# Kernel tuning notes

Measured on AMD Instinct MI355X. Metric: run time of the kernel, lower is better.

Reference implementation:

```python
import jax, jax.numpy as jnp
import numpy as np

B, S, F, H = 64, 1024, 128, 512  # batch, seq_len, features, lstm units


def setup_inputs() -> dict:
    key = jax.random.key(0)
    k1, k2, k3 = jax.random.split(key, 3)
    x = jax.random.normal(k1, (B, S, F), dtype=jnp.float32)
    # Keras LSTM params: kernel [F, 4H], recurrent_kernel [H, 4H], bias [4H]
    W = jax.random.normal(k2, (F, 4 * H), dtype=jnp.float32) * (1.0 / np.sqrt(F))
    U = jax.random.normal(k3, (H, 4 * H), dtype=jnp.float32) * (1.0 / np.sqrt(H))
    b = jnp.zeros((4 * H,), dtype=jnp.float32)
    return {"x": x, "W": W, "U": U, "b": b}


def _lstm_relu(x, W, U, b):
    # Precompute input projection for all timesteps: [B,S,4H]
    xW = jnp.einsum("bsf,fg->bsg", x, W) + b
    xW_t = jnp.transpose(xW, (1, 0, 2))  # [S,B,4H] for scan over time
    h0 = jnp.zeros((x.shape[0], H), dtype=x.dtype)
    c0 = jnp.zeros((x.shape[0], H), dtype=x.dtype)

    def step(carry, xw):
        h, c = carry
        z = xw + h @ U  # [B,4H]
        zi, zf, zg, zo = jnp.split(z, 4, axis=-1)  # Keras gate order i,f,c,o
        i = jax.nn.sigmoid(zi)
        f = jax.nn.sigmoid(zf)
        g = jax.nn.relu(zg)          # activation='relu' (candidate)
        o = jax.nn.sigmoid(zo)
        c_new = f * c + i * g
        h_new = o * jax.nn.relu(c_new)  # activation='relu' (output)
        return (h_new, c_new), h_new

    _, hs = jax.lax.scan(step, (h0, c0), xW_t)
    return jnp.transpose(hs, (1, 0, 2))  # [B,S,H]


def reference(x, W, U, b):
    # LSTM(return_sequences=True, activation='relu'); Dropout inactive at inference.
    return _lstm_relu(x, W, U, b)
```

## Files before the change

kernel.cpp:

```cpp
#include <hip/hip_runtime.h>
#include <stdint.h>


#define S_ 1024
#define F_ 128
#define H_ 512
#define G4_ 2048
#define SLOTS 32
#define KH 16
#define LDKS 640
#define HB (64 * H_)

typedef __attribute__((ext_vector_type(8))) short short8;
typedef __attribute__((ext_vector_type(4))) float f32x4;
typedef unsigned long long ull;

__device__ __forceinline__ unsigned short f2bf(float f) {
  union { float f; unsigned u; } v; v.f = f;
  unsigned u = v.u + 0x7fffu + ((v.u >> 16) & 1u);
  return (unsigned short)(u >> 16);
}

__device__ __forceinline__ short8 pack2(f32x4 a, f32x4 b) {
  short8 r;
#pragma unroll
  for (int i = 0; i < 4; ++i) r[i] = (short)f2bf(a[i]);
#pragma unroll
  for (int i = 0; i < 4; ++i) r[4 + i] = (short)f2bf(b[i]);
  return r;
}

__device__ __forceinline__ int swz(int cc, int k) {
  return (cc * LDKS + k) ^ ((cc & 7) << 3);
}

__global__ __launch_bounds__(256, 1) void lstm_pers(
    const float* __restrict__ x, const float* __restrict__ W,
    const float* __restrict__ U, const float* __restrict__ bias,
    float* __restrict__ out, unsigned int* ws_sync, unsigned short* hbuf) {

  __shared__ unsigned short V[64 * LDKS];
  __shared__ f32x4 R[3][4][64];
  __shared__ int meta[2];

  const int tid  = threadIdx.x;
  const int w    = tid >> 6;
  const int lane = tid & 63;
  const int l15  = lane & 15;
  const int l4   = lane >> 4;
  const int koff = l4 * 8;

  if (tid == 0) {
    unsigned int xcc;
    asm volatile("s_getreg_b32 %0, hwreg(20, 0, 4)" : "=s"(xcc));
    xcc &= 7;
    unsigned sv = atomicAdd(ws_sync + xcc * 32, 1u);
    meta[0] = (int)xcc;
    meta[1] = (int)(sv & 31);
  }
  __syncthreads();
  const int xcc  = meta[0];
  const int slot = meta[1];

  unsigned int* flags  = ws_sync + 256;
  unsigned int* gflags = flags + xcc * SLOTS * 16;
  unsigned int* myflag = gflags + slot * 16;
  unsigned int* pollp  = gflags + (lane & 31) * 16;

  const int u0    = slot * 16;
  const int bbase = xcc * 8;

  for (int idx = tid; idx < (64 * LDKS) / 4; idx += 256) {
    const int q4   = idx & 15;
    const int k    = idx >> 4;
    const int gate = q4 & 3;
    const int ul0  = (q4 >> 2) * 4;
    const int col  = gate * H_ + u0 + ul0;
    const float* src = (k < H_) ? (U + (size_t)k * G4_ + col)
                                : (W + (size_t)(k - H_) * G4_ + col);
    const f32x4 v4 = *(const f32x4*)src;
#pragma unroll
    for (int q = 0; q < 4; ++q) {
      const int ul = ul0 + q;
      const int cc = (ul >> 2) * 16 + (ul & 3) * 4 + gate;
      V[swz(cc, k)] = f2bf(v4[q]);
    }
  }

  float bias_r[4][4];
  if (w == 0) {
#pragma unroll
    for (int tl = 0; tl < 4; ++tl)
#pragma unroll
      for (int g = 0; g < 4; ++g)
        bias_r[tl][g] = bias[g * H_ + u0 + tl * 4 + l4];
  }

  __syncthreads();

  const int brow = bbase + (l15 & 7);
  const float* xrow = x + (size_t)brow * S_ * F_ + koff + w * 32;
  const unsigned short* hrow0 = hbuf + (size_t)brow * H_ + koff;

  float cst[4] = {0.f, 0.f, 0.f, 0.f};

  for (int t = 0; t < S_; ++t) {
    const float* xt = xrow + (size_t)t * F_;
    const f32x4 xa = *(const f32x4*)(xt);
    const f32x4 xb = *(const f32x4*)(xt + 4);

    if (t > 0 && w == 0) {
      const unsigned tgt = (unsigned)t;
      while (true) {
        unsigned v = __hip_atomic_load(pollp, __ATOMIC_RELAXED, __HIP_MEMORY_SCOPE_AGENT);
        if (__all((int)(v >= tgt))) break;
      }
    }
    __syncthreads();

    short8 bh[4];
    if (t > 0) {
      const unsigned short* hr = hrow0 + (size_t)(t & 1) * HB;
#pragma unroll
      for (int i = 0; i < 4; ++i) {
        union { ull u[2]; short8 s; } bb;
        const ull* hq = (const ull*)(hr + (4 * w + i) * 32);
        bb.u[0] = __hip_atomic_load(hq,     __ATOMIC_RELAXED, __HIP_MEMORY_SCOPE_AGENT);
        bb.u[1] = __hip_atomic_load(hq + 1, __ATOMIC_RELAXED, __HIP_MEMORY_SCOPE_AGENT);
        bh[i] = bb.s;
      }
    }

    f32x4 acc[4];
#pragma unroll
    for (int tl = 0; tl < 4; ++tl) {
      f32x4 a;
      if (w == 0) {
        a[0] = bias_r[tl][0]; a[1] = bias_r[tl][1];
        a[2] = bias_r[tl][2]; a[3] = bias_r[tl][3];
      } else {
        a[0] = 0.f; a[1] = 0.f; a[2] = 0.f; a[3] = 0.f;
      }
      acc[tl] = a;
    }

    {
      const short8 bx = pack2(xa, xb);
      const int k0 = (KH + w) * 32 + koff;
#pragma unroll
      for (int tl = 0; tl < 4; ++tl) {
        const short8 a = *(const short8*)&V[swz(tl * 16 + l15, k0)];
        acc[tl] = __builtin_amdgcn_mfma_f32_16x16x32_bf16(a, bx, acc[tl], 0, 0, 0);
      }
    }

    if (t > 0) {
#pragma unroll
      for (int i = 0; i < 4; ++i) {
        const int k0 = (4 * w + i) * 32 + koff;
#pragma unroll
        for (int tl = 0; tl < 4; ++tl) {
          const short8 a = *(const short8*)&V[swz(tl * 16 + l15, k0)];
          acc[tl] = __builtin_amdgcn_mfma_f32_16x16x32_bf16(a, bh[i], acc[tl], 0, 0, 0);
        }
      }
    }

    if (w > 0) {
#pragma unroll
      for (int tl = 0; tl < 4; ++tl) R[w - 1][tl][lane] = acc[tl];
    }
    __syncthreads();

    if (w == 0) {
#pragma unroll
      for (int ww = 0; ww < 3; ++ww)
#pragma unroll
        for (int tl = 0; tl < 4; ++tl) {
          const f32x4 r = R[ww][tl][lane];
          acc[tl][0] += r[0]; acc[tl][1] += r[1];
          acc[tl][2] += r[2]; acc[tl][3] += r[3];
        }

      unsigned short* hw = hbuf + (size_t)((t + 1) & 1) * HB + (size_t)brow * H_;
      float* orow = out + ((size_t)brow * S_ + t) * H_;
      float hv[4];
#pragma unroll
      for (int tl = 0; tl < 4; ++tl) {
        const float zi = acc[tl][0], zf = acc[tl][1], zg = acc[tl][2], zo = acc[tl][3];
        const float ig = 1.f / (1.f + __expf(-zi));
        const float fg = 1.f / (1.f + __expf(-zf));
        const float gg = fmaxf(zg, 0.f);
        const float og = 1.f / (1.f + __expf(-zo));
        const float cn = fg * cst[tl] + ig * gg;
        cst[tl] = cn;
        hv[tl] = og * fmaxf(cn, 0.f);
        if (l15 < 8) hw[u0 + tl * 4 + l4] = f2bf(hv[tl]);
      }

      asm volatile("s_waitcnt vmcnt(0)" ::: "memory");
      if (lane == 0)
        __hip_atomic_store(myflag, (unsigned)(t + 1), __ATOMIC_RELAXED, __HIP_MEMORY_SCOPE_AGENT);
      if (l15 < 8) {
#pragma unroll
        for (int tl = 0; tl < 4; ++tl)
          orow[u0 + tl * 4 + l4] = hv[tl];
      }
    }
  }
}

extern "C" void kernel_launch(void* const* d_in, const int* in_sizes, int n_in,
                              void* d_out, int out_size, void* d_ws, size_t ws_size,
                              hipStream_t stream) {
  const float* x = (const float*)d_in[0];
  const float* W = (const float*)d_in[1];
  const float* U = (const float*)d_in[2];
  const float* b = (const float*)d_in[3];
  float* out = (float*)d_out;

  unsigned int*   ws_sync = (unsigned int*)d_ws;
  unsigned short* hbuf    = (unsigned short*)((char*)d_ws + 32768);

  hipMemsetAsync(d_ws, 0, 32768, stream);

  lstm_pers<<<dim3(256), dim3(256), 0, stream>>>(x, W, U, b, out, ws_sync, hbuf);
}
```

Baseline: 3.030 ms.

## Distribute gate epilogue across all waves, prefetch x, pack flags in one line

```diff
diff --git a/kernel.cpp b/kernel.cpp
--- a/kernel.cpp
+++ b/kernel.cpp
@@ -40,7 +40,7 @@
     float* __restrict__ out, unsigned int* ws_sync, unsigned short* hbuf) {
 
   __shared__ unsigned short V[64 * LDKS];
-  __shared__ f32x4 R[3][4][64];
+  __shared__ f32x4 R[4][4][64];
   __shared__ int meta[2];
 
   const int tid  = threadIdx.x;
@@ -63,9 +63,9 @@
   const int slot = meta[1];
 
   unsigned int* flags  = ws_sync + 256;
-  unsigned int* gflags = flags + xcc * SLOTS * 16;
-  unsigned int* myflag = gflags + slot * 16;
-  unsigned int* pollp  = gflags + (lane & 31) * 16;
+  unsigned int* gline  = flags + xcc * 32;
+  unsigned int* myflag = gline + slot;
+  unsigned int* pollp  = gline + (lane & 31);
 
   const int u0    = slot * 16;
   const int bbase = xcc * 8;
@@ -87,27 +87,42 @@
     }
   }
 
-  float bias_r[4][4];
-  if (w == 0) {
-#pragma unroll
-    for (int tl = 0; tl < 4; ++tl)
-#pragma unroll
-      for (int g = 0; g < 4; ++g)
-        bias_r[tl][g] = bias[g * H_ + u0 + tl * 4 + l4];
-  }
+  float bias_r[4];
+#pragma unroll
+  for (int g = 0; g < 4; ++g) bias_r[g] = bias[g * H_ + u0 + w * 4 + l4];
 
   __syncthreads();
 
   const int brow = bbase + (l15 & 7);
   const float* xrow = x + (size_t)brow * S_ * F_ + koff + w * 32;
   const unsigned short* hrow0 = hbuf + (size_t)brow * H_ + koff;
-
-  float cst[4] = {0.f, 0.f, 0.f, 0.f};
+  const int myunit = u0 + w * 4 + l4;
+
+  float cst = 0.f;
+
+  f32x4 xa = *(const f32x4*)(xrow);
+  f32x4 xb = *(const f32x4*)(xrow + 4);
 
   for (int t = 0; t < S_; ++t) {
-    const float* xt = xrow + (size_t)t * F_;
-    const f32x4 xa = *(const f32x4*)(xt);
-    const f32x4 xb = *(const f32x4*)(xt + 4);
+    f32x4 acc[4];
+#pragma unroll
+    for (int tl = 0; tl < 4; ++tl) { acc[tl][0]=0.f; acc[tl][1]=0.f; acc[tl][2]=0.f; acc[tl][3]=0.f; }
+    {
+      const short8 bx = pack2(xa, xb);
+      const int k0 = (KH + w) * 32 + koff;
+#pragma unroll
+      for (int tl = 0; tl < 4; ++tl) {
+        const short8 a = *(const short8*)&V[swz(tl * 16 + l15, k0)];
+        acc[tl] = __builtin_amdgcn_mfma_f32_16x16x32_bf16(a, bx, acc[tl], 0, 0, 0);
+      }
+    }
+
+    {
+      const int tn = (t + 1 < S_) ? t + 1 : t;
+      const float* xt = xrow + (size_t)tn * F_;
+      xa = *(const f32x4*)(xt);
+      xb = *(const f32x4*)(xt + 4);
+    }
 
     if (t > 0 && w == 0) {
       const unsigned tgt = (unsigned)t;
@@ -118,9 +133,9 @@
     }
     __syncthreads();
 
-    short8 bh[4];
     if (t > 0) {
       const unsigned short* hr = hrow0 + (size_t)(t & 1) * HB;
+      short8 bh[4];
 #pragma unroll
       for (int i = 0; i < 4; ++i) {
         union { ull u[2]; short8 s; } bb;
@@ -129,32 +144,6 @@
         bb.u[1] = __hip_atomic_load(hq + 1, __ATOMIC_RELAXED, __HIP_MEMORY_SCOPE_AGENT);
         bh[i] = bb.s;
       }
-    }
-
-    f32x4 acc[4];
-#pragma unroll
-    for (int tl = 0; tl < 4; ++tl) {
-      f32x4 a;
-      if (w == 0) {
-        a[0] = bias_r[tl][0]; a[1] = bias_r[tl][1];
-        a[2] = bias_r[tl][2]; a[3] = bias_r[tl][3];
-      } else {
-        a[0] = 0.f; a[1] = 0.f; a[2] = 0.f; a[3] = 0.f;
-      }
-      acc[tl] = a;
-    }
-
-    {
-      const short8 bx = pack2(xa, xb);
-      const int k0 = (KH + w) * 32 + koff;
-#pragma unroll
-      for (int tl = 0; tl < 4; ++tl) {
-        const short8 a = *(const short8*)&V[swz(tl * 16 + l15, k0)];
-        acc[tl] = __builtin_amdgcn_mfma_f32_16x16x32_bf16(a, bx, acc[tl], 0, 0, 0);
-      }
-    }
-
-    if (t > 0) {
 #pragma unroll
       for (int i = 0; i < 4; ++i) {
         const int k0 = (4 * w + i) * 32 + koff;
@@ -166,47 +155,35 @@
       }
     }
 
-    if (w > 0) {
-#pragma unroll
-      for (int tl = 0; tl < 4; ++tl) R[w - 1][tl][lane] = acc[tl];
-    }
+#pragma unroll
+    for (int tl = 0; tl < 4; ++tl) R[w][tl][lane] = acc[tl];
     __syncthreads();
 
-    if (w == 0) {
-#pragma unroll
-      for (int ww = 0; ww < 3; ++ww)
-#pragma unroll
-        for (int tl = 0; tl < 4; ++tl) {
-          const f32x4 r = R[ww][tl][lane];
-          acc[tl][0] += r[0]; acc[tl][1] += r[1];
-          acc[tl][2] += r[2]; acc[tl][3] += r[3];
-        }
-
-      unsigned short* hw = hbuf + (size_t)((t + 1) & 1) * HB + (size_t)brow * H_;
-      float* orow = out + ((size_t)brow * S_ + t) * H_;
-      float hv[4];
-#pragma unroll
-      for (int tl = 0; tl < 4; ++tl) {
-        const float zi = acc[tl][0], zf = acc[tl][1], zg = acc[tl][2], zo = acc[tl][3];
-        const float ig = 1.f / (1.f + __expf(-zi));
-        const float fg = 1.f / (1.f + __expf(-zf));
-        const float gg = fmaxf(zg, 0.f);
-        const float og = 1.f / (1.f + __expf(-zo));
-        const float cn = fg * cst[tl] + ig * gg;
-        cst[tl] = cn;
-        hv[tl] = og * fmaxf(cn, 0.f);
-        if (l15 < 8) hw[u0 + tl * 4 + l4] = f2bf(hv[tl]);
-      }
-
-      asm volatile("s_waitcnt vmcnt(0)" ::: "memory");
-      if (lane == 0)
-        __hip_atomic_store(myflag, (unsigned)(t + 1), __ATOMIC_RELAXED, __HIP_MEMORY_SCOPE_AGENT);
-      if (l15 < 8) {
-#pragma unroll
-        for (int tl = 0; tl < 4; ++tl)
-          orow[u0 + tl * 4 + l4] = hv[tl];
-      }
-    }
+    f32x4 z;
+    {
+      const f32x4 r0 = R[0][w][lane], r1 = R[1][w][lane],
+                  r2 = R[2][w][lane], r3 = R[3][w][lane];
+#pragma unroll
+      for (int g = 0; g < 4; ++g)
+        z[g] = bias_r[g] + r0[g] + r1[g] + r2[g] + r3[g];
+    }
+
+    const float ig = 1.f / (1.f + __expf(-z[0]));
+    const float fg = 1.f / (1.f + __expf(-z[1]));
+    const float gg = fmaxf(z[2], 0.f);
+    const float og = 1.f / (1.f + __expf(-z[3]));
+    const float cn = fg * cst + ig * gg;
+    cst = cn;
+    const float hv = og * fmaxf(cn, 0.f);
+
+    if (l15 < 8)
+      hbuf[(size_t)((t + 1) & 1) * HB + (size_t)brow * H_ + myunit] = f2bf(hv);
+    asm volatile("s_waitcnt vmcnt(0)" ::: "memory");
+    __syncthreads();
+    if (tid == 0)
+      __hip_atomic_store(myflag, (unsigned)(t + 1), __ATOMIC_RELAXED, __HIP_MEMORY_SCOPE_AGENT);
+    if (l15 < 8)
+      out[((size_t)brow * S_ + t) * H_ + myunit] = hv;
   }
 }
 
```

New measurement: 2.627 ms. 13.3% less time.
